# Optimization experiments

Measured on AMD Instinct MI355X. Metric: run time of the kernel, lower is better.

The kernel has to match this reference:

```python
import jax, jax.numpy as jnp
import numpy as np
import math

B, S, H = 8, 160, 768
DEP = 64
NH, DH = 12, H // 12
W_EDGE = 1.0
EPS = 1e-5


def setup_inputs() -> dict:
    key = jax.random.key(0)
    ks = jax.random.split(key, 16)
    sc_h = 1.0 / math.sqrt(H)
    sc_d = 1.0 / math.sqrt(DEP)
    return {
        "token_feature": jax.random.normal(ks[0], (B, S, H), jnp.float32),
        "edge_feature": jax.random.normal(ks[1], (B, S, S, DEP), jnp.float32),
        "dependency_masks": jax.random.randint(ks[2], (B, S, S), 0, 2, jnp.int32),
        "Wq": jax.random.normal(ks[3], (H, H), jnp.float32) * sc_h,
        "bq": jnp.zeros((H,), jnp.float32),
        "Wk": jax.random.normal(ks[4], (H, H), jnp.float32) * sc_h,
        "bk": jnp.zeros((H,), jnp.float32),
        "Wv": jax.random.normal(ks[5], (H, H), jnp.float32) * sc_h,
        "bv": jnp.zeros((H,), jnp.float32),
        "Wek": jax.random.normal(ks[6], (DEP, H), jnp.float32) * sc_d,
        "bek": jnp.zeros((H,), jnp.float32),
        "Wev": jax.random.normal(ks[7], (DEP, H), jnp.float32) * sc_d,
        "bev": jnp.zeros((H,), jnp.float32),
        "ln_g": jnp.ones((H,), jnp.float32),
        "ln_b": jnp.zeros((H,), jnp.float32),
    }


def _heads3(x):  # [B,S,H] -> [B,NH,S,DH]
    return x.reshape(B, S, NH, DH).transpose(0, 2, 1, 3)


def _heads4(x):  # [B,S,S,H] -> [B,NH,S,S,DH]
    return x.reshape(B, S, S, NH, DH).transpose(0, 3, 1, 2, 4)


def reference(token_feature, edge_feature, dependency_masks,
              Wq, bq, Wk, bk, Wv, bv, Wek, bek, Wev, bev, ln_g, ln_b):
    q = _heads3(token_feature @ Wq + bq)   # [B,NH,S,DH]
    k = _heads3(token_feature @ Wk + bk)
    v = _heads3(token_feature @ Wv + bv)
    ek = _heads4(edge_feature @ Wek + bek)  # [B,NH,S,S,DH]
    ev = _heads4(edge_feature @ Wev + bev)
    # key_ij = k_j + w*ek_ij ; scores_ij = q_i . key_ij / sqrt(dh)
    scores = (jnp.einsum('bhid,bhjd->bhij', q, k)
              + W_EDGE * jnp.einsum('bhid,bhijd->bhij', q, ek))
    scores = scores / math.sqrt(DH)
    mask = (dependency_masks[:, None, :, :] == 0)  # [B,1,S,S]
    scores = jnp.where(mask, jnp.float32(-10000.0), scores)
    probs = jax.nn.softmax(scores, axis=-1)  # dropout is identity in eval
    ctx = (jnp.einsum('bhij,bhjd->bhid', probs, v)
           + W_EDGE * jnp.einsum('bhij,bhijd->bhid', probs, ev))
    ctx = ctx.transpose(0, 2, 1, 3).reshape(B, S, H)
    x = token_feature + ctx
    mu = jnp.mean(x, axis=-1, keepdims=True)
    var = jnp.mean(jnp.square(x - mu), axis=-1, keepdims=True)
    return (x - mu) / jnp.sqrt(var + EPS) * ln_g + ln_b
```

## Files before the change

kernel.cpp:

```cpp
#include <hip/hip_runtime.h>
#include <hip/hip_bf16.h>
#include <math.h>

#define BB 8
#define SS 160
#define HH 768
#define DEPTH 64
#define NHEAD 12
#define DHEAD 64
#define BS (BB*SS)

constexpr float EPS_C = 1e-5f;

typedef __attribute__((ext_vector_type(8))) short bf16x8;
typedef __attribute__((ext_vector_type(4))) float f32x4;

__global__ __launch_bounds__(256) void cast_x(
    const float* __restrict__ X, __hip_bfloat16* __restrict__ Xb)
{
    int idx = blockIdx.x * 256 + threadIdx.x;
    float4 xin = ((const float4*)X)[idx];
    __hip_bfloat16* o = Xb + (size_t)idx * 4;
    o[0] = __float2bfloat16(xin.x); o[1] = __float2bfloat16(xin.y);
    o[2] = __float2bfloat16(xin.z); o[3] = __float2bfloat16(xin.w);
}

__global__ __launch_bounds__(256) void transpose_cast_w(
    const float* __restrict__ Wq, const float* __restrict__ Wk,
    const float* __restrict__ Wv, __hip_bfloat16* __restrict__ WT)
{
    __shared__ float t[32][33];
    const float* W = (blockIdx.z == 0) ? Wq : (blockIdx.z == 1) ? Wk : Wv;
    __hip_bfloat16* o = WT + (size_t)blockIdx.z * HH * HH;
    int kt = blockIdx.x * 32, nt = blockIdx.y * 32;
    int tx = threadIdx.x & 31, ty = threadIdx.x >> 5;
#pragma unroll
    for (int r = 0; r < 32; r += 8)
        t[ty + r][tx] = W[(size_t)(kt + ty + r) * HH + nt + tx];
    __syncthreads();
#pragma unroll
    for (int r = 0; r < 32; r += 8)
        o[(size_t)(nt + ty + r) * HH + kt + tx] = __float2bfloat16(t[tx][ty + r]);
}

__global__ __launch_bounds__(256) void gemm_qkv(
    const __hip_bfloat16* __restrict__ Xb, const __hip_bfloat16* __restrict__ WT,
    const float* __restrict__ bq, const float* __restrict__ bk,
    const float* __restrict__ bv,
    __hip_bfloat16* __restrict__ qb, __hip_bfloat16* __restrict__ kb,
    __hip_bfloat16* __restrict__ vb)
{
    __shared__ int4 sA[4][128];
    __shared__ int4 sB[4][64];
    int m0 = blockIdx.x * 128, n0 = blockIdx.y * 64, mat = blockIdx.z;
    const short* X = (const short*)Xb;
    const short* W = (const short*)WT + (size_t)mat * HH * HH;
    const float* bias = (mat == 0) ? bq : (mat == 1) ? bk : bv;
    int tid = threadIdx.x, w = tid >> 6, l = tid & 63;
    int wm = (w >> 1) * 64, wn = (w & 1) * 32;
    int khalf = l >> 4, lc = l & 15;

    f32x4 acc[4][2];
#pragma unroll
    for (int i = 0; i < 4; i++)
#pragma unroll
        for (int j = 0; j < 2; j++) acc[i][j] = (f32x4){0.f, 0.f, 0.f, 0.f};

    for (int k0 = 0; k0 < HH; k0 += 32) {
        __syncthreads();
        sA[w][l]      = *(const int4*)(X + (size_t)(m0 + l) * HH + k0 + w * 8);
        sA[w][l + 64] = *(const int4*)(X + (size_t)(m0 + l + 64) * HH + k0 + w * 8);
        sB[w][l]      = *(const int4*)(W + (size_t)(n0 + l) * HH + k0 + w * 8);
        __syncthreads();
        bf16x8 b0 = *(const bf16x8*)&sB[khalf][wn + lc];
        bf16x8 b1 = *(const bf16x8*)&sB[khalf][wn + 16 + lc];
#pragma unroll
        for (int mi = 0; mi < 4; mi++) {
            bf16x8 a = *(const bf16x8*)&sA[khalf][wm + mi * 16 + lc];
            acc[mi][0] = __builtin_amdgcn_mfma_f32_16x16x32_bf16(a, b0, acc[mi][0], 0, 0, 0);
            acc[mi][1] = __builtin_amdgcn_mfma_f32_16x16x32_bf16(a, b1, acc[mi][1], 0, 0, 0);
        }
    }

    int rg = (l >> 4) * 4;
    __hip_bfloat16* outm = (mat == 0) ? qb : (mat == 1) ? kb : vb;
#pragma unroll
    for (int ni = 0; ni < 2; ni++) {
        int gcol = n0 + wn + ni * 16 + lc;
        float bv_ = bias[gcol];
#pragma unroll
        for (int mi = 0; mi < 4; mi++) {
            int grow = m0 + wm + mi * 16 + rg;
            f32x4 a = acc[mi][ni];
            __hip_bfloat16* o = outm + (size_t)grow * HH + gcol;
            o[0]      = __float2bfloat16(a.x + bv_);
            o[HH]     = __float2bfloat16(a.y + bv_);
            o[2 * HH] = __float2bfloat16(a.z + bv_);
            o[3 * HH] = __float2bfloat16(a.w + bv_);
        }
    }
}

__global__ __launch_bounds__(256) void scores_gemm(
    const __hip_bfloat16* __restrict__ qb, const __hip_bfloat16* __restrict__ kb,
    _Float16* __restrict__ sc)
{
    __shared__ int4 sQ[8][160];
    __shared__ int4 sK[8][160];
    int h = blockIdx.x, b = blockIdx.y;
    const short* Q = (const short*)qb + (size_t)b * SS * HH + h * DHEAD;
    const short* K = (const short*)kb + (size_t)b * SS * HH + h * DHEAD;
    int tid = threadIdx.x, w = tid >> 6, l = tid & 63;

    for (int idx = tid; idx < SS * 8; idx += 256) {
        int row = idx >> 3, ch = idx & 7;
        sQ[ch][row] = *(const int4*)(Q + (size_t)row * HH + ch * 8);
        sK[ch][row] = *(const int4*)(K + (size_t)row * HH + ch * 8);
    }
    __syncthreads();

    int wm = (w >> 1) * 80, wn = (w & 1) * 80;
    int khalf = l >> 4, lc = l & 15;
    f32x4 acc[5][5];
#pragma unroll
    for (int i = 0; i < 5; i++)
#pragma unroll
        for (int j = 0; j < 5; j++) acc[i][j] = (f32x4){0.f, 0.f, 0.f, 0.f};

#pragma unroll
    for (int s = 0; s < 2; s++) {
        int c = s * 4 + khalf;
        bf16x8 bf[5];
#pragma unroll
        for (int ni = 0; ni < 5; ni++)
            bf[ni] = *(const bf16x8*)&sK[c][wn + ni * 16 + lc];
#pragma unroll
        for (int mi = 0; mi < 5; mi++) {
            bf16x8 a = *(const bf16x8*)&sQ[c][wm + mi * 16 + lc];
#pragma unroll
            for (int ni = 0; ni < 5; ni++)
                acc[mi][ni] = __builtin_amdgcn_mfma_f32_16x16x32_bf16(a, bf[ni], acc[mi][ni], 0, 0, 0);
        }
    }

    int rg = (l >> 4) * 4;
    _Float16* base = sc + (size_t)(b * NHEAD + h) * SS * SS;
#pragma unroll
    for (int mi = 0; mi < 5; mi++) {
        int i0 = wm + mi * 16 + rg;
#pragma unroll
        for (int ni = 0; ni < 5; ni++) {
            int j = wn + ni * 16 + lc;
            f32x4 a = acc[mi][ni];
            base[(size_t)(i0 + 0) * SS + j] = (_Float16)(a.x * 0.125f);
            base[(size_t)(i0 + 1) * SS + j] = (_Float16)(a.y * 0.125f);
            base[(size_t)(i0 + 2) * SS + j] = (_Float16)(a.z * 0.125f);
            base[(size_t)(i0 + 3) * SS + j] = (_Float16)(a.w * 0.125f);
        }
    }
}

__global__ __launch_bounds__(256) void attn_kernel(
    const float* __restrict__ token, const float* __restrict__ edge,
    const int* __restrict__ mask,
    const __hip_bfloat16* __restrict__ q_ws, const _Float16* __restrict__ sc,
    const __hip_bfloat16* __restrict__ v_ws,
    const float* __restrict__ Wek, const float* __restrict__ bek,
    const float* __restrict__ Wev, const float* __restrict__ bev,
    const float* __restrict__ ln_g, const float* __restrict__ ln_b,
    float* __restrict__ out)
{
    __shared__ float  s_q[HH];
    __shared__ float  s_qek[NHEAD * DEPTH];
    __shared__ float  s_qbek[NHEAD];
    __shared__ float  s_pool[32 * 66];
    __shared__ float  s_scores[NHEAD][SS];
    __shared__ float  s_pe[NHEAD][DEPTH];
    __shared__ int    s_mask[SS];
    __shared__ float  s_red[8];

    int bi = blockIdx.x;
    int b  = bi / SS;
    int i  = bi - b * SS;
    int tid = threadIdx.x;
    int w = tid >> 6, l = tid & 63;

    for (int c = tid; c < HH; c += 256)
        s_q[c] = __bfloat162float(q_ws[(size_t)bi * HH + c]);
    if (tid < SS) s_mask[tid] = mask[(size_t)bi * SS + tid];
    __syncthreads();

#pragma unroll
    for (int round = 0; round < 12; round++) {
        int lid = round * 256 + tid;
        int oidx = lid >> 2;
        int h = oidx >> 6, d = oidx & 63;
        int c0 = (lid & 3) << 4;
        const float* wp = Wek + (size_t)d * HH + h * DHEAD + c0;
        const float* qp = s_q + h * DHEAD + c0;
        float sum = 0.f;
#pragma unroll
        for (int cc = 0; cc < 16; cc += 4) {
            float4 wv = *(const float4*)(wp + cc);
            float4 qv = *(const float4*)(qp + cc);
            sum += qv.x * wv.x + qv.y * wv.y + qv.z * wv.z + qv.w * wv.w;
        }
        sum += __shfl_xor(sum, 1, 64);
        sum += __shfl_xor(sum, 2, 64);
        if ((lid & 3) == 0) s_qek[oidx] = sum;
    }
    if (tid < NHEAD) {
        const float* qp = s_q + tid * DHEAD;
        const float* bp = bek + tid * DHEAD;
        float sum = 0.f;
#pragma unroll
        for (int c = 0; c < DHEAD; c++) sum += qp[c] * bp[c];
        s_qbek[tid] = sum;
    }

    const float* e_row = edge + (size_t)bi * SS * DEPTH;
    const _Float16* scp = sc + (size_t)b * NHEAD * SS * SS + (size_t)i * SS;

    for (int jt = 0; jt < SS; jt += 32) {
        __syncthreads();
        for (int idx = tid; idx < 32 * 32; idx += 256) {
            int jj = idx >> 5, dd = idx & 31;
            *(float2*)(&s_pool[jj * 66 + dd * 2]) =
                *(const float2*)(e_row + (size_t)(jt + jj) * DEPTH + dd * 2);
        }
        __syncthreads();
        for (int item = tid; item < 32 * NHEAD; item += 256) {
            int jj = item & 31, h = item >> 5;
            int j = jt + jj;
            float qk = (float)scp[(size_t)h * (SS * SS) + j];
            const float* qekp = s_qek + h * DHEAD;
            const float* ep   = s_pool + jj * 66;
            float sum2 = 0.f;
#pragma unroll
            for (int d = 0; d < DHEAD; d += 4) {
                float4 qe = *(const float4*)(qekp + d);
                float2 e0 = *(const float2*)(ep + d);
                float2 e1 = *(const float2*)(ep + d + 2);
                sum2 += qe.x * e0.x + qe.y * e0.y + qe.z * e1.x + qe.w * e1.y;
            }
            s_scores[h][j] = s_mask[j] ? qk + (sum2 + s_qbek[h]) * 0.125f
                                       : -10000.0f;
        }
    }
    __syncthreads();

    for (int h = w; h < NHEAD; h += 4) {
        float v0 = s_scores[h][l];
        float v1 = s_scores[h][l + 64];
        float v2 = (l < 32) ? s_scores[h][l + 128] : -INFINITY;
        float mx = fmaxf(v0, fmaxf(v1, v2));
#pragma unroll
        for (int mm = 32; mm >= 1; mm >>= 1) mx = fmaxf(mx, __shfl_xor(mx, mm, 64));
        float e0 = expf(v0 - mx), e1 = expf(v1 - mx);
        float e2 = (l < 32) ? expf(v2 - mx) : 0.f;
        float sm = e0 + e1 + e2;
#pragma unroll
        for (int mm = 32; mm >= 1; mm >>= 1) sm += __shfl_xor(sm, mm, 64);
        float inv = 1.0f / sm;
        s_scores[h][l]      = e0 * inv;
        s_scores[h][l + 64] = e1 * inv;
        if (l < 32) s_scores[h][l + 128] = e2 * inv;
    }
    __syncthreads();

    {
        int h0 = w * 3;
        float av0 = 0.f, av1 = 0.f, av2 = 0.f;
        float pe0 = 0.f, pe1 = 0.f, pe2 = 0.f;
        const __hip_bfloat16* vbp = v_ws + (size_t)b * SS * HH + h0 * DHEAD + l;
        const float* er = e_row + l;
        const float* p0r = &s_scores[h0][0];
        const float* p1r = &s_scores[h0 + 1][0];
        const float* p2r = &s_scores[h0 + 2][0];
#pragma unroll 4
        for (int j = 0; j < SS; j++) {
            float p0 = p0r[j], p1 = p1r[j], p2 = p2r[j];
            const __hip_bfloat16* vp = vbp + (size_t)j * HH;
            av0 += p0 * __bfloat162float(vp[0]);
            av1 += p1 * __bfloat162float(vp[DHEAD]);
            av2 += p2 * __bfloat162float(vp[2 * DHEAD]);
            float ev = er[(size_t)j * DEPTH];
            pe0 += p0 * ev; pe1 += p1 * ev; pe2 += p2 * ev;
        }
        s_pe[h0][l]     = pe0;
        s_pe[h0 + 1][l] = pe1;
        s_pe[h0 + 2][l] = pe2;
        s_q[h0 * DHEAD + l]       = av0;
        s_q[(h0 + 1) * DHEAD + l] = av1;
        s_q[(h0 + 2) * DHEAD + l] = av2;
    }
    __syncthreads();

    float* s_x = s_pool;
    for (int mdx = tid; mdx < HH; mdx += 256) {
        int h = mdx >> 6;
        const float* pep = &s_pe[h][0];
        float sum = 0.f;
#pragma unroll
        for (int d = 0; d < DEPTH; d++) sum += pep[d] * Wev[(size_t)d * HH + mdx];
        float ctx = s_q[mdx] + (sum + bev[mdx]);
        s_x[mdx] = token[(size_t)bi * HH + mdx] + ctx;
    }
    __syncthreads();

    float lsum = 0.f, lsq = 0.f;
    for (int c = tid; c < HH; c += 256) {
        float x = s_x[c];
        lsum += x; lsq += x * x;
    }
#pragma unroll
    for (int mm = 32; mm >= 1; mm >>= 1) {
        lsum += __shfl_xor(lsum, mm, 64);
        lsq  += __shfl_xor(lsq,  mm, 64);
    }
    if (l == 0) { s_red[w] = lsum; s_red[4 + w] = lsq; }
    __syncthreads();
    float tsum = s_red[0] + s_red[1] + s_red[2] + s_red[3];
    float tsq  = s_red[4] + s_red[5] + s_red[6] + s_red[7];
    float mu  = tsum / HH;
    float var = tsq / HH - mu * mu;
    float rstd = rsqrtf(var + EPS_C);
    for (int c = tid; c < HH; c += 256)
        out[(size_t)bi * HH + c] = (s_x[c] - mu) * rstd * ln_g[c] + ln_b[c];
}

extern "C" void kernel_launch(void* const* d_in, const int* in_sizes, int n_in,
                              void* d_out, int out_size, void* d_ws, size_t ws_size,
                              hipStream_t stream) {
    const float* token = (const float*)d_in[0];
    const float* edge  = (const float*)d_in[1];
    const int*   mask  = (const int*)d_in[2];
    const float* Wq = (const float*)d_in[3];  const float* bq = (const float*)d_in[4];
    const float* Wk = (const float*)d_in[5];  const float* bk = (const float*)d_in[6];
    const float* Wv = (const float*)d_in[7];  const float* bv = (const float*)d_in[8];
    const float* Wek = (const float*)d_in[9];  const float* bek = (const float*)d_in[10];
    const float* Wev = (const float*)d_in[11]; const float* bev = (const float*)d_in[12];
    const float* ln_g = (const float*)d_in[13]; const float* ln_b = (const float*)d_in[14];
    float* out = (float*)d_out;

    __hip_bfloat16* qb = (__hip_bfloat16*)d_ws;
    __hip_bfloat16* kb = qb + (size_t)BS * HH;
    __hip_bfloat16* vb = kb + (size_t)BS * HH;
    __hip_bfloat16* Xb = vb + (size_t)BS * HH;
    __hip_bfloat16* WT = Xb + (size_t)BS * HH;
    _Float16*       sc = (_Float16*)Xb;

    cast_x<<<(BS * HH / 4) / 256, 256, 0, stream>>>(token, Xb);
    transpose_cast_w<<<dim3(24, 24, 3), 256, 0, stream>>>(Wq, Wk, Wv, WT);
    gemm_qkv<<<dim3(BS / 128, HH / 64, 3), 256, 0, stream>>>(
        Xb, WT, bq, bk, bv, qb, kb, vb);
    scores_gemm<<<dim3(NHEAD, BB), 256, 0, stream>>>(qb, kb, sc);
    attn_kernel<<<BS, 256, 0, stream>>>(token, edge, mask, qb, sc, vb,
                                        Wek, bek, Wev, bev, ln_g, ln_b, out);
}
```

Baseline: 135.8 us.

## Move q·Wek and edge-score terms out of attention into MFMA kernels

Takes the per-row q·Wek projection and the edge-score dot products out of the attention kernel. They now run in two new kernels that use bf16 MFMA instructions: qek_gemm writes qek into the k buffer, which is free by then, and escore_add adds the scaled edge term into the fp16 score matrix. The attention kernel now only reads the finished scores plus the bias term, which cuts its shared memory and scalar FMA work. In exchange there are two extra launches, the edge tensor is read an extra time, and the edge features and the score accumulation lose precision (bf16 and fp16).

```diff
diff --git a/kernel.cpp b/kernel.cpp
--- a/kernel.cpp
+++ b/kernel.cpp
@@ -14,6 +14,12 @@
 
 typedef __attribute__((ext_vector_type(8))) short bf16x8;
 typedef __attribute__((ext_vector_type(4))) float f32x4;
+
+__device__ inline short f2bs(float x) {
+    union { __hip_bfloat16 b; short s; } u;
+    u.b = __float2bfloat16(x);
+    return u.s;
+}
 
 __global__ __launch_bounds__(256) void cast_x(
     const float* __restrict__ X, __hip_bfloat16* __restrict__ Xb)
@@ -160,22 +166,103 @@
     }
 }
 
+__global__ __launch_bounds__(256) void qek_gemm(
+    const __hip_bfloat16* __restrict__ qb, const float* __restrict__ Wek,
+    __hip_bfloat16* __restrict__ qek)
+{
+    int task = blockIdx.x * 4 + (threadIdx.x >> 6);
+    int l = threadIdx.x & 63;
+    int mt = task / NHEAD, h = task - mt * NHEAD;
+    int bi0 = mt * 16;
+    int lr = l & 15, kg = l >> 4;
+    const short* Q = (const short*)qb;
+
+    bf16x8 a0 = *(const bf16x8*)(Q + (size_t)(bi0 + lr) * HH + h * DHEAD + kg * 8);
+    bf16x8 a1 = *(const bf16x8*)(Q + (size_t)(bi0 + lr) * HH + h * DHEAD + 32 + kg * 8);
+
+    short* O = (short*)qek;
+#pragma unroll
+    for (int nt = 0; nt < 4; nt++) {
+        int d = nt * 16 + lr;
+        const float* wp = Wek + (size_t)d * HH + h * DHEAD + kg * 8;
+        float4 w0 = *(const float4*)(wp);
+        float4 w1 = *(const float4*)(wp + 4);
+        float4 w2 = *(const float4*)(wp + 32);
+        float4 w3 = *(const float4*)(wp + 36);
+        bf16x8 b0, b1;
+        b0[0]=f2bs(w0.x); b0[1]=f2bs(w0.y); b0[2]=f2bs(w0.z); b0[3]=f2bs(w0.w);
+        b0[4]=f2bs(w1.x); b0[5]=f2bs(w1.y); b0[6]=f2bs(w1.z); b0[7]=f2bs(w1.w);
+        b1[0]=f2bs(w2.x); b1[1]=f2bs(w2.y); b1[2]=f2bs(w2.z); b1[3]=f2bs(w2.w);
+        b1[4]=f2bs(w3.x); b1[5]=f2bs(w3.y); b1[6]=f2bs(w3.z); b1[7]=f2bs(w3.w);
+        f32x4 acc = (f32x4){0.f, 0.f, 0.f, 0.f};
+        acc = __builtin_amdgcn_mfma_f32_16x16x32_bf16(a0, b0, acc, 0, 0, 0);
+        acc = __builtin_amdgcn_mfma_f32_16x16x32_bf16(a1, b1, acc, 0, 0, 0);
+        int row0 = bi0 + kg * 4;
+#pragma unroll
+        for (int r = 0; r < 4; r++)
+            O[(size_t)(row0 + r) * HH + h * DHEAD + nt * 16 + lr] = f2bs(acc[r]);
+    }
+}
+
+__global__ __launch_bounds__(256) void escore_add(
+    const float* __restrict__ edge, const __hip_bfloat16* __restrict__ qek,
+    _Float16* __restrict__ sc)
+{
+    int bi = blockIdx.x * 4 + (threadIdx.x >> 6);
+    int l = threadIdx.x & 63;
+    int b = bi / SS, i = bi - b * SS;
+    int lr = l & 15, kg = l >> 4;
+    const short* QE = (const short*)qek + (size_t)bi * HH;
+
+    bf16x8 qe0 = *(const bf16x8*)(QE + lr * DHEAD + kg * 8);
+    bf16x8 qe1 = *(const bf16x8*)(QE + lr * DHEAD + 32 + kg * 8);
+
+    const float* E = edge + (size_t)bi * SS * DEPTH;
+    int h = lr, hc = (h < NHEAD) ? h : (NHEAD - 1);
+    bool hvalid = (h < NHEAD);
+    _Float16* srow = sc + ((size_t)(b * NHEAD + hc) * SS + i) * SS;
+
+#pragma unroll 2
+    for (int jt = 0; jt < 10; jt++) {
+        const float* ep = E + (size_t)(jt * 16 + lr) * DEPTH + kg * 8;
+        float4 e0 = *(const float4*)(ep);
+        float4 e1 = *(const float4*)(ep + 4);
+        float4 e2 = *(const float4*)(ep + 32);
+        float4 e3 = *(const float4*)(ep + 36);
+        bf16x8 a0, a1;
+        a0[0]=f2bs(e0.x); a0[1]=f2bs(e0.y); a0[2]=f2bs(e0.z); a0[3]=f2bs(e0.w);
+        a0[4]=f2bs(e1.x); a0[5]=f2bs(e1.y); a0[6]=f2bs(e1.z); a0[7]=f2bs(e1.w);
+        a1[0]=f2bs(e2.x); a1[1]=f2bs(e2.y); a1[2]=f2bs(e2.z); a1[3]=f2bs(e2.w);
+        a1[4]=f2bs(e3.x); a1[5]=f2bs(e3.y); a1[6]=f2bs(e3.z); a1[7]=f2bs(e3.w);
+        f32x4 acc = (f32x4){0.f, 0.f, 0.f, 0.f};
+        acc = __builtin_amdgcn_mfma_f32_16x16x32_bf16(a0, qe0, acc, 0, 0, 0);
+        acc = __builtin_amdgcn_mfma_f32_16x16x32_bf16(a1, qe1, acc, 0, 0, 0);
+        if (hvalid) {
+            int j0 = jt * 16 + kg * 4;
+            _Float16* p = srow + j0;
+            p[0] = (_Float16)((float)p[0] + 0.125f * acc[0]);
+            p[1] = (_Float16)((float)p[1] + 0.125f * acc[1]);
+            p[2] = (_Float16)((float)p[2] + 0.125f * acc[2]);
+            p[3] = (_Float16)((float)p[3] + 0.125f * acc[3]);
+        }
+    }
+}
+
 __global__ __launch_bounds__(256) void attn_kernel(
     const float* __restrict__ token, const float* __restrict__ edge,
     const int* __restrict__ mask,
     const __hip_bfloat16* __restrict__ q_ws, const _Float16* __restrict__ sc,
     const __hip_bfloat16* __restrict__ v_ws,
-    const float* __restrict__ Wek, const float* __restrict__ bek,
+    const float* __restrict__ bek,
     const float* __restrict__ Wev, const float* __restrict__ bev,
     const float* __restrict__ ln_g, const float* __restrict__ ln_b,
     float* __restrict__ out)
 {
     __shared__ float  s_q[HH];
-    __shared__ float  s_qek[NHEAD * DEPTH];
-    __shared__ float  s_qbek[NHEAD];
-    __shared__ float  s_pool[32 * 66];
     __shared__ float  s_scores[NHEAD][SS];
     __shared__ float  s_pe[NHEAD][DEPTH];
+    __shared__ float  s_x[HH];
+    __shared__ float  s_qbek[NHEAD];
     __shared__ int    s_mask[SS];
     __shared__ float  s_red[8];
 
@@ -190,25 +277,6 @@
     if (tid < SS) s_mask[tid] = mask[(size_t)bi * SS + tid];
     __syncthreads();
 
-#pragma unroll
-    for (int round = 0; round < 12; round++) {
-        int lid = round * 256 + tid;
-        int oidx = lid >> 2;
-        int h = oidx >> 6, d = oidx & 63;
-        int c0 = (lid & 3) << 4;
-        const float* wp = Wek + (size_t)d * HH + h * DHEAD + c0;
-        const float* qp = s_q + h * DHEAD + c0;
-        float sum = 0.f;
-#pragma unroll
-        for (int cc = 0; cc < 16; cc += 4) {
-            float4 wv = *(const float4*)(wp + cc);
-            float4 qv = *(const float4*)(qp + cc);
-            sum += qv.x * wv.x + qv.y * wv.y + qv.z * wv.z + qv.w * wv.w;
-        }
-        sum += __shfl_xor(sum, 1, 64);
-        sum += __shfl_xor(sum, 2, 64);
-        if ((lid & 3) == 0) s_qek[oidx] = sum;
-    }
     if (tid < NHEAD) {
         const float* qp = s_q + tid * DHEAD;
         const float* bp = bek + tid * DHEAD;
@@ -217,35 +285,13 @@
         for (int c = 0; c < DHEAD; c++) sum += qp[c] * bp[c];
         s_qbek[tid] = sum;
     }
-
-    const float* e_row = edge + (size_t)bi * SS * DEPTH;
-    const _Float16* scp = sc + (size_t)b * NHEAD * SS * SS + (size_t)i * SS;
-
-    for (int jt = 0; jt < SS; jt += 32) {
-        __syncthreads();
-        for (int idx = tid; idx < 32 * 32; idx += 256) {
-            int jj = idx >> 5, dd = idx & 31;
-            *(float2*)(&s_pool[jj * 66 + dd * 2]) =
-                *(const float2*)(e_row + (size_t)(jt + jj) * DEPTH + dd * 2);
-        }
-        __syncthreads();
-        for (int item = tid; item < 32 * NHEAD; item += 256) {
-            int jj = item & 31, h = item >> 5;
-            int j = jt + jj;
-            float qk = (float)scp[(size_t)h * (SS * SS) + j];
-            const float* qekp = s_qek + h * DHEAD;
-            const float* ep   = s_pool + jj * 66;
-            float sum2 = 0.f;
-#pragma unroll
-            for (int d = 0; d < DHEAD; d += 4) {
-                float4 qe = *(const float4*)(qekp + d);
-                float2 e0 = *(const float2*)(ep + d);
-                float2 e1 = *(const float2*)(ep + d + 2);
-                sum2 += qe.x * e0.x + qe.y * e0.y + qe.z * e1.x + qe.w * e1.y;
-            }
-            s_scores[h][j] = s_mask[j] ? qk + (sum2 + s_qbek[h]) * 0.125f
-                                       : -10000.0f;
-        }
+    __syncthreads();
+
+    const _Float16* scp = sc + (size_t)(b * NHEAD) * (SS * SS) + (size_t)i * SS;
+    for (int idx = tid; idx < NHEAD * SS; idx += 256) {
+        int h = idx / SS, j = idx - h * SS;
+        float qk = (float)scp[(size_t)h * (SS * SS) + j];
+        s_scores[h][j] = s_mask[j] ? (qk + 0.125f * s_qbek[h]) : -10000.0f;
     }
     __syncthreads();
 
@@ -268,6 +314,7 @@
     }
     __syncthreads();
 
+    const float* e_row = edge + (size_t)bi * SS * DEPTH;
     {
         int h0 = w * 3;
         float av0 = 0.f, av1 = 0.f, av2 = 0.f;
@@ -296,7 +343,6 @@
     }
     __syncthreads();
 
-    float* s_x = s_pool;
     for (int mdx = tid; mdx < HH; mdx += 256) {
         int h = mdx >> 6;
         const float* pep = &s_pe[h][0];
@@ -349,12 +395,15 @@
     __hip_bfloat16* Xb = vb + (size_t)BS * HH;
     __hip_bfloat16* WT = Xb + (size_t)BS * HH;
     _Float16*       sc = (_Float16*)Xb;
+    __hip_bfloat16* qek = kb;
 
     cast_x<<<(BS * HH / 4) / 256, 256, 0, stream>>>(token, Xb);
     transpose_cast_w<<<dim3(24, 24, 3), 256, 0, stream>>>(Wq, Wk, Wv, WT);
     gemm_qkv<<<dim3(BS / 128, HH / 64, 3), 256, 0, stream>>>(
         Xb, WT, bq, bk, bv, qb, kb, vb);
     scores_gemm<<<dim3(NHEAD, BB), 256, 0, stream>>>(qb, kb, sc);
+    qek_gemm<<<240, 256, 0, stream>>>(qb, Wek, qek);
+    escore_add<<<BS / 4, 256, 0, stream>>>(edge, qek, sc);
     attn_kernel<<<BS, 256, 0, stream>>>(token, edge, mask, qb, sc, vb,
-                                        Wek, bek, Wev, bev, ln_g, ln_b, out);
-}
+                                        bek, Wev, bev, ln_g, ln_b, out);
+}
```

After: 108.9 us. 19.8% less time.
